# Kernel tuning notes

Measured on AMD Instinct MI355X. Metric: run time of the kernel, lower is better.

Reference implementation:

```python
import jax, jax.numpy as jnp
import numpy as np

B, N, C = 2, 100000, 256
H, D, S = 8, 64, 64
INNER = H * D

def setup_inputs() -> dict:
    key = jax.random.key(0)
    ks = jax.random.split(key, 5)
    x = jax.random.normal(ks[0], (B, N, C), dtype=jnp.float32)
    W_x = jax.random.normal(ks[1], (C, INNER), dtype=jnp.float32) / np.sqrt(C)
    b_x = jnp.zeros((INNER,), dtype=jnp.float32)
    W_fx = jax.random.normal(ks[2], (C, INNER), dtype=jnp.float32) / np.sqrt(C)
    b_fx = jnp.zeros((INNER,), dtype=jnp.float32)
    W_slice = jax.random.normal(ks[3], (D, S), dtype=jnp.float32) / np.sqrt(D)
    b_slice = jnp.zeros((S,), dtype=jnp.float32)
    temperature = jnp.ones((1, 1, H, 1), dtype=jnp.float32) * 0.5
    return {"x": x, "W_x": W_x, "b_x": b_x, "W_fx": W_fx, "b_fx": b_fx,
            "W_slice": W_slice, "b_slice": b_slice, "temperature": temperature}

def reference(x, W_x, b_x, W_fx, b_fx, W_slice, b_slice, temperature):
    b, n, _ = x.shape
    # linear projections to (B, N, H, D)
    px = (x @ W_x + b_x).reshape(b, n, H, D)   # query-like projection
    fx = (x @ W_fx + b_fx).reshape(b, n, H, D) # feature (value) projection
    # slice logits (B, N, H, S)
    slice_proj = jnp.einsum('bnhd,ds->bnhs', px, W_slice) + b_slice
    temp = jnp.clip(temperature, 0.1, 5.0)     # (1,1,H,1), broadcast over S
    slice_weights = jax.nn.softmax(slice_proj / temp, axis=-1)  # (B,N,H,S)
    slice_norm = slice_weights.sum(axis=1)     # (B,H,S)
    # weighted aggregation of tokens into slice tokens (B,H,S,D)
    slice_token = jnp.einsum('bnhs,bnhd->bhsd', slice_weights, fx)
    slice_token = slice_token / (slice_norm[..., None] + 1e-5)
    return slice_token
```

## Files before the change

### kernel.cpp

```cpp
#include <hip/hip_runtime.h>
#include <hip/hip_bf16.h>
#include <cstdint>

#define B_     2
#define N_     100000
#define C_     256
#define H_     8
#define D_     64
#define S_     64
#define INNER_ 512

#define TILE_T 64
#define NTILES ((N_ + TILE_T - 1) / TILE_T)
#define PBLK   32

#define WEFFT_OFF 0
#define WFXT_OFF  262144
#define BIASE_OFF 524288
#define SLAB_OFF  526336
#define NSLAB_OFF (SLAB_OFF + B_*H_*PBLK*4096*4)
#define WS_BIG_END (NSLAB_OFF + B_*H_*PBLK*64*4)
#define ACC_OFF   526336
#define NRM_OFF   (ACC_OFF + B_*H_*S_*D_*4)
#define WS_SMALL_END (NRM_OFF + B_*H_*S_*4)

typedef __attribute__((ext_vector_type(8))) short short8;
typedef __attribute__((ext_vector_type(4))) float f32x4;

__device__ inline short f2bf(float f) {
    __hip_bfloat16 h = __float2bfloat16(f);
    short s; __builtin_memcpy(&s, &h, 2); return s;
}
__device__ inline uint32_t pk2(float a, float b) {
    __hip_bfloat162 h = __float22bfloat162_rn(float2{a, b});
    uint32_t u; __builtin_memcpy(&u, &h, 4); return u;
}

__global__ void prep_kernel(const float* __restrict__ W_x,
                            const float* __restrict__ b_x,
                            const float* __restrict__ W_fx,
                            const float* __restrict__ W_slice,
                            const float* __restrict__ b_slice,
                            const float* __restrict__ temperature,
                            uint8_t* __restrict__ wsb) {
    int wid  = (blockIdx.x * 256 + threadIdx.x) >> 6;
    int lane = threadIdx.x & 63;
    if (wid < H_ * C_) {
        int h = wid >> 8, k = wid & 255;
        float t = temperature[h]; t = fminf(fmaxf(t, 0.1f), 5.0f);
        float sc = 1.44269504088896f / t;
        const float* wx = W_x + k * INNER_ + h * 64;
        float a = 0.f;
        #pragma unroll 8
        for (int d = 0; d < D_; ++d)
            a = fmaf(wx[d], W_slice[d * 64 + lane], a);
        ((short*)(wsb + WEFFT_OFF))[(h * 64 + lane) * 256 + k] = f2bf(a * sc);
    } else if (wid < 2 * H_ * C_) {
        int j = wid - H_ * C_;
        int h = j >> 8, k = j & 255;
        ((short*)(wsb + WFXT_OFF))[(h * 64 + lane) * 256 + k] =
            f2bf(W_fx[k * INNER_ + h * 64 + lane]);
    } else if (wid < 2 * H_ * C_ + H_) {
        int h = wid - 2 * H_ * C_;
        float t = temperature[h]; t = fminf(fmaxf(t, 0.1f), 5.0f);
        float sc = 1.44269504088896f / t;
        float a = 0.f;
        #pragma unroll 8
        for (int d = 0; d < D_; ++d)
            a = fmaf(b_x[h * 64 + d], W_slice[d * 64 + lane], a);
        ((float*)(wsb + BIASE_OFF))[h * 64 + lane] = (a + b_slice[lane]) * sc;
    }
}

template<bool SLAB>
__global__ __launch_bounds__(512, 4) void main_kernel(
        const float* __restrict__ x,
        const float* __restrict__ b_fx,
        const uint8_t* __restrict__ wsb,
        float* __restrict__ accg,
        float* __restrict__ nrmg) {
    __shared__ union {
        short xs[TILE_T * 264];
        struct { short wsl[S_ * 72]; short fsl[D_ * 72]; } wf;
    } u;
    __shared__ float smB[TILE_T * 4];

    const int tid = threadIdx.x;
    const int bid = blockIdx.x;
    const int cc = bid & 7;
    const int h  = (bid >> 3) & 7;
    const int pb = (bid >> 6) * 8 + cc;
    const int p  = pb & 31;
    const int b  = pb >> 5;

    const int lane = tid & 63, wv = tid >> 6;
    const int l = lane & 15, q = lane >> 4;
    const int g  = wv >> 2;
    const int w4 = wv & 3;

    const short* wT = (const short*)(wsb + (g ? WFXT_OFF : WEFFT_OFF)) + h * (64 * 256);
    short8 breg[8];
    #pragma unroll
    for (int k = 0; k < 8; ++k)
        breg[k] = *(const short8*)(wT + (w4 * 16 + l) * 256 + k * 32 + q * 8);

    const float bias_n = g ? b_fx[h * 64 + w4 * 16 + l]
                           : ((const float*)(wsb + BIASE_OFF))[h * 64 + w4 * 16 + l];

    const float* xb = x + (size_t)b * ((size_t)N_ * C_);
    f32x4 accO[2] = {};
    float nrmacc = 0.f;

    float4 xv[8];
    {
        const int col = lane * 4;
        #pragma unroll
        for (int j = 0; j < 8; ++j) {
            int gt = p * TILE_T + wv + 8 * j;
            xv[j] = (gt < N_) ? *(const float4*)(xb + (size_t)gt * C_ + col)
                              : float4{0.f, 0.f, 0.f, 0.f};
        }
    }

    #pragma unroll 1
    for (int tile = p; tile < NTILES; tile += PBLK) {
        __syncthreads();
        {
            #pragma unroll
            for (int j = 0; j < 8; ++j) {
                int row = wv + 8 * j;
                uint2 pk = { pk2(xv[j].x, xv[j].y), pk2(xv[j].z, xv[j].w) };
                *(uint2*)(u.xs + row * 264 + lane * 4) = pk;
            }
        }
        __syncthreads();

        {
            int nxt = tile + PBLK;
            if (nxt < NTILES) {
                const int col = lane * 4;
                #pragma unroll
                for (int j = 0; j < 8; ++j) {
                    int gt = nxt * TILE_T + wv + 8 * j;
                    xv[j] = (gt < N_) ? *(const float4*)(xb + (size_t)gt * C_ + col)
                                      : float4{0.f, 0.f, 0.f, 0.f};
                }
            }
        }

        f32x4 acc[4] = {};
        #pragma unroll
        for (int k = 0; k < 8; ++k) {
            #pragma unroll
            for (int m = 0; m < 4; ++m) {
                short8 a = *(const short8*)(u.xs + (m * 16 + l) * 264 + k * 32 + q * 8);
                acc[m] = __builtin_amdgcn_mfma_f32_16x16x32_bf16(a, breg[k], acc[m], 0, 0, 0);
            }
        }

        if (g == 0) {
            #pragma unroll
            for (int m = 0; m < 4; ++m)
                #pragma unroll
                for (int r = 0; r < 4; ++r) {
                    float e = __builtin_amdgcn_exp2f(acc[m][r] + bias_n);
                    acc[m][r] = e;
                    float sv = e;
                    sv += __shfl_xor(sv, 1, 64);
                    sv += __shfl_xor(sv, 2, 64);
                    sv += __shfl_xor(sv, 4, 64);
                    sv += __shfl_xor(sv, 8, 64);
                    if (l == 0) smB[(m * 16 + q * 4 + r) * 4 + wv] = sv;
                }
        } else {
            #pragma unroll
            for (int m = 0; m < 4; ++m)
                #pragma unroll
                for (int r = 0; r < 4; ++r)
                    acc[m][r] += bias_n;
        }
        __syncthreads();

        const int t0 = tile * TILE_T;
        if (g == 0) {
            #pragma unroll
            for (int m = 0; m < 4; ++m) {
                #pragma unroll
                for (int r = 0; r < 4; ++r) {
                    int tok = m * 16 + q * 4 + r;
                    float4 s4 = *(const float4*)(smB + tok * 4);
                    float S = (s4.x + s4.y) + (s4.z + s4.w);
                    float f = __builtin_amdgcn_rcpf(S);
                    if (t0 + tok >= N_) f = 0.f;
                    float w = acc[m][r] * f;
                    acc[m][r] = w;
                    nrmacc += w;
                }
                uint2 pk = { pk2(acc[m][0], acc[m][1]), pk2(acc[m][2], acc[m][3]) };
                *(uint2*)(u.wf.wsl + (w4 * 16 + l) * 72 + m * 16 + q * 4) = pk;
            }
        } else {
            #pragma unroll
            for (int m = 0; m < 4; ++m) {
                uint2 pk = { pk2(acc[m][0], acc[m][1]), pk2(acc[m][2], acc[m][3]) };
                *(uint2*)(u.wf.fsl + (w4 * 16 + l) * 72 + m * 16 + q * 4) = pk;
            }
        }
        __syncthreads();

        #pragma unroll
        for (int kk = 0; kk < 2; ++kk) {
            short8 aw = *(const short8*)(u.wf.wsl + (w4 * 16 + l) * 72 + kk * 32 + q * 8);
            #pragma unroll
            for (int nt = 0; nt < 2; ++nt) {
                short8 bf = *(const short8*)(u.wf.fsl + (g * 32 + nt * 16 + l) * 72 + kk * 32 + q * 8);
                accO[nt] = __builtin_amdgcn_mfma_f32_16x16x32_bf16(aw, bf, accO[nt], 0, 0, 0);
            }
        }
    }

    if (SLAB) {
        float* sp = accg + ((size_t)(b * H_ + h) * PBLK + p) * 4096;
        #pragma unroll
        for (int nt = 0; nt < 2; ++nt)
            #pragma unroll
            for (int r = 0; r < 4; ++r)
                sp[(w4 * 16 + q * 4 + r) * 64 + g * 32 + nt * 16 + l] = accO[nt][r];
        if (g == 0) {
            float v = nrmacc;
            v += __shfl_xor(v, 16, 64);
            v += __shfl_xor(v, 32, 64);
            if (lane < 16)
                nrmg[((b * H_ + h) * PBLK + p) * 64 + w4 * 16 + lane] = v;
        }
    } else {
        float* ag = accg + (size_t)((b * H_ + h) * 64) * 64;
        #pragma unroll
        for (int nt = 0; nt < 2; ++nt)
            #pragma unroll
            for (int r = 0; r < 4; ++r)
                atomicAdd(ag + (w4 * 16 + q * 4 + r) * 64 + g * 32 + nt * 16 + l, accO[nt][r]);
        if (g == 0) {
            float v = nrmacc;
            v += __shfl_xor(v, 16, 64);
            v += __shfl_xor(v, 32, 64);
            if (lane < 16)
                atomicAdd(nrmg + (b * H_ + h) * 64 + w4 * 16 + lane, v);
        }
    }
}

__global__ void finalize_big(const float* __restrict__ slab,
                             const float* __restrict__ nslab,
                             float* __restrict__ out) {
    int idx = blockIdx.x * 256 + threadIdx.x;
    int bh = idx >> 12, sd = idx & 4095, s = sd >> 6;
    const float* sp = slab  + (size_t)bh * PBLK * 4096 + sd;
    const float* np = nslab + bh * PBLK * 64 + s;
    float acc = 0.f, nn = 0.f;
    #pragma unroll 8
    for (int p = 0; p < PBLK; ++p) { acc += sp[p * 4096]; nn += np[p * 64]; }
    out[idx] = acc / (nn + 1e-5f);
}

__global__ void finalize_small(const uint8_t* __restrict__ wsb, float* __restrict__ out) {
    int idx = blockIdx.x * 256 + threadIdx.x;
    float a = ((const float*)(wsb + ACC_OFF))[idx];
    float n = ((const float*)(wsb + NRM_OFF))[idx / D_];
    out[idx] = a / (n + 1e-5f);
}

extern "C" void kernel_launch(void* const* d_in, const int* in_sizes, int n_in,
                              void* d_out, int out_size, void* d_ws, size_t ws_size,
                              hipStream_t stream) {
    const float* x           = (const float*)d_in[0];
    const float* W_x         = (const float*)d_in[1];
    const float* b_x         = (const float*)d_in[2];
    const float* W_fx        = (const float*)d_in[3];
    const float* b_fx        = (const float*)d_in[4];
    const float* W_slice     = (const float*)d_in[5];
    const float* b_slice     = (const float*)d_in[6];
    const float* temperature = (const float*)d_in[7];
    float* out = (float*)d_out;
    uint8_t* wsb = (uint8_t*)d_ws;

    int prep_waves = 2 * H_ * C_ + H_;
    prep_kernel<<<dim3((prep_waves + 3) / 4), dim3(256), 0, stream>>>(
        W_x, b_x, W_fx, W_slice, b_slice, temperature, wsb);

    if (ws_size >= (size_t)WS_BIG_END) {
        main_kernel<true><<<dim3(PBLK * H_ * B_), dim3(512), 0, stream>>>(
            x, b_fx, wsb, (float*)(wsb + SLAB_OFF), (float*)(wsb + NSLAB_OFF));
        finalize_big<<<dim3(256), dim3(256), 0, stream>>>(
            (const float*)(wsb + SLAB_OFF), (const float*)(wsb + NSLAB_OFF), out);
    } else {
        hipMemsetAsync(wsb + ACC_OFF, 0, (B_ * H_ * S_ * D_ + B_ * H_ * S_) * 4, stream);
        main_kernel<false><<<dim3(PBLK * H_ * B_), dim3(512), 0, stream>>>(
            x, b_fx, wsb, (float*)(wsb + ACC_OFF), (float*)(wsb + NRM_OFF));
        finalize_small<<<dim3(256), dim3(256), 0, stream>>>(wsb, out);
    }
}
```

Baseline: 574.9 us.

## Switch main kernel to 32x32x16 MFMA tiles with split-K output reduction

Replaces the 16x16x32 MFMA tiling with 32x32x16 MFMAs in both the projection GEMM and the slice-aggregation GEMM. Each wave now computes a 32x32 block, and the aggregation is split over K across the two wave groups, followed by an in-LDS reduction at the end. The weighted and feature slices get their own shared buffers instead of aliasing the x tile, which removes one barrier per tile. This is meant to cut LDS A-operand reads and instruction count. In exchange it uses more registers (launch bounds drop to 2 blocks per SIMD) and adds an epilogue reduction through shared memory.

```diff
diff --git a/kernel.cpp b/kernel.cpp
--- a/kernel.cpp
+++ b/kernel.cpp
@@ -24,8 +24,9 @@
 #define NRM_OFF   (ACC_OFF + B_*H_*S_*D_*4)
 #define WS_SMALL_END (NRM_OFF + B_*H_*S_*4)
 
-typedef __attribute__((ext_vector_type(8))) short short8;
-typedef __attribute__((ext_vector_type(4))) float f32x4;
+typedef __attribute__((ext_vector_type(8)))  short short8;
+typedef __attribute__((ext_vector_type(4)))  float f32x4;
+typedef __attribute__((ext_vector_type(16))) float f32x16;
 
 __device__ inline short f2bf(float f) {
     __hip_bfloat16 h = __float2bfloat16(f);
@@ -73,7 +74,7 @@
 }
 
 template<bool SLAB>
-__global__ __launch_bounds__(512, 4) void main_kernel(
+__global__ __launch_bounds__(512, 2) void main_kernel(
         const float* __restrict__ x,
         const float* __restrict__ b_fx,
         const uint8_t* __restrict__ wsb,
@@ -81,9 +82,11 @@
         float* __restrict__ nrmg) {
     __shared__ union {
         short xs[TILE_T * 264];
-        struct { short wsl[S_ * 72]; short fsl[D_ * 72]; } wf;
+        struct { float eg[4][64][16]; float np[4][64]; } fin;
     } u;
-    __shared__ float smB[TILE_T * 4];
+    __shared__ short wsl[S_ * 72];
+    __shared__ short fsl[D_ * 72];
+    __shared__ float smB[TILE_T * 2];
 
     const int tid = threadIdx.x;
     const int bid = blockIdx.x;
@@ -94,21 +97,23 @@
     const int b  = pb >> 5;
 
     const int lane = tid & 63, wv = tid >> 6;
-    const int l = lane & 15, q = lane >> 4;
+    const int l31 = lane & 31, hh = lane >> 5;
     const int g  = wv >> 2;
-    const int w4 = wv & 3;
+    const int mh = (wv >> 1) & 1;
+    const int nh = wv & 1;
+    const int kh = g, sh = mh, dh = nh;
 
     const short* wT = (const short*)(wsb + (g ? WFXT_OFF : WEFFT_OFF)) + h * (64 * 256);
-    short8 breg[8];
+    short8 breg[16];
     #pragma unroll
-    for (int k = 0; k < 8; ++k)
-        breg[k] = *(const short8*)(wT + (w4 * 16 + l) * 256 + k * 32 + q * 8);
-
-    const float bias_n = g ? b_fx[h * 64 + w4 * 16 + l]
-                           : ((const float*)(wsb + BIASE_OFF))[h * 64 + w4 * 16 + l];
+    for (int kk = 0; kk < 16; ++kk)
+        breg[kk] = *(const short8*)(wT + (nh * 32 + l31) * 256 + kk * 16 + hh * 8);
+
+    const float bias_n = g ? b_fx[h * 64 + nh * 32 + l31]
+                           : ((const float*)(wsb + BIASE_OFF))[h * 64 + nh * 32 + l31];
 
     const float* xb = x + (size_t)b * ((size_t)N_ * C_);
-    f32x4 accO[2] = {};
+    f32x16 accO = {};
     float nrmacc = 0.f;
 
     float4 xv[8];
@@ -124,14 +129,11 @@
 
     #pragma unroll 1
     for (int tile = p; tile < NTILES; tile += PBLK) {
-        __syncthreads();
-        {
-            #pragma unroll
-            for (int j = 0; j < 8; ++j) {
-                int row = wv + 8 * j;
-                uint2 pk = { pk2(xv[j].x, xv[j].y), pk2(xv[j].z, xv[j].w) };
-                *(uint2*)(u.xs + row * 264 + lane * 4) = pk;
-            }
+        #pragma unroll
+        for (int j = 0; j < 8; ++j) {
+            int row = wv + 8 * j;
+            uint2 pk = { pk2(xv[j].x, xv[j].y), pk2(xv[j].z, xv[j].w) };
+            *(uint2*)(u.xs + row * 264 + lane * 4) = pk;
         }
         __syncthreads();
 
@@ -148,105 +150,104 @@
             }
         }
 
-        f32x4 acc[4] = {};
-        #pragma unroll
-        for (int k = 0; k < 8; ++k) {
-            #pragma unroll
-            for (int m = 0; m < 4; ++m) {
-                short8 a = *(const short8*)(u.xs + (m * 16 + l) * 264 + k * 32 + q * 8);
-                acc[m] = __builtin_amdgcn_mfma_f32_16x16x32_bf16(a, breg[k], acc[m], 0, 0, 0);
-            }
+        f32x16 acc = {};
+        #pragma unroll
+        for (int kk = 0; kk < 16; ++kk) {
+            short8 a = *(const short8*)(u.xs + (mh * 32 + l31) * 264 + kk * 16 + hh * 8);
+            acc = __builtin_amdgcn_mfma_f32_32x32x16_bf16(a, breg[kk], acc, 0, 0, 0);
         }
 
         if (g == 0) {
             #pragma unroll
-            for (int m = 0; m < 4; ++m)
-                #pragma unroll
-                for (int r = 0; r < 4; ++r) {
-                    float e = __builtin_amdgcn_exp2f(acc[m][r] + bias_n);
-                    acc[m][r] = e;
-                    float sv = e;
-                    sv += __shfl_xor(sv, 1, 64);
-                    sv += __shfl_xor(sv, 2, 64);
-                    sv += __shfl_xor(sv, 4, 64);
-                    sv += __shfl_xor(sv, 8, 64);
-                    if (l == 0) smB[(m * 16 + q * 4 + r) * 4 + wv] = sv;
-                }
-        } else {
-            #pragma unroll
-            for (int m = 0; m < 4; ++m)
-                #pragma unroll
-                for (int r = 0; r < 4; ++r)
-                    acc[m][r] += bias_n;
-        }
-        __syncthreads();
-
-        const int t0 = tile * TILE_T;
-        if (g == 0) {
-            #pragma unroll
-            for (int m = 0; m < 4; ++m) {
-                #pragma unroll
-                for (int r = 0; r < 4; ++r) {
-                    int tok = m * 16 + q * 4 + r;
-                    float4 s4 = *(const float4*)(smB + tok * 4);
-                    float S = (s4.x + s4.y) + (s4.z + s4.w);
-                    float f = __builtin_amdgcn_rcpf(S);
-                    if (t0 + tok >= N_) f = 0.f;
-                    float w = acc[m][r] * f;
-                    acc[m][r] = w;
-                    nrmacc += w;
-                }
-                uint2 pk = { pk2(acc[m][0], acc[m][1]), pk2(acc[m][2], acc[m][3]) };
-                *(uint2*)(u.wf.wsl + (w4 * 16 + l) * 72 + m * 16 + q * 4) = pk;
+            for (int r = 0; r < 16; ++r) {
+                float e = __builtin_amdgcn_exp2f(acc[r] + bias_n);
+                acc[r] = e;
+                float s = e;
+                s += __shfl_xor(s, 1, 64);
+                s += __shfl_xor(s, 2, 64);
+                s += __shfl_xor(s, 4, 64);
+                s += __shfl_xor(s, 8, 64);
+                s += __shfl_xor(s, 16, 64);
+                if (l31 == 0)
+                    smB[(mh * 32 + (r & 3) + 8 * (r >> 2) + hh * 4) * 2 + nh] = s;
             }
         } else {
             #pragma unroll
-            for (int m = 0; m < 4; ++m) {
-                uint2 pk = { pk2(acc[m][0], acc[m][1]), pk2(acc[m][2], acc[m][3]) };
-                *(uint2*)(u.wf.fsl + (w4 * 16 + l) * 72 + m * 16 + q * 4) = pk;
+            for (int r = 0; r < 16; ++r) acc[r] += bias_n;
+            #pragma unroll
+            for (int rq = 0; rq < 4; ++rq) {
+                uint2 pk = { pk2(acc[rq * 4 + 0], acc[rq * 4 + 1]),
+                             pk2(acc[rq * 4 + 2], acc[rq * 4 + 3]) };
+                *(uint2*)(fsl + (nh * 32 + l31) * 72 + mh * 32 + rq * 8 + hh * 4) = pk;
             }
         }
         __syncthreads();
 
+        if (g == 0) {
+            const int t0 = tile * TILE_T;
+            #pragma unroll
+            for (int rq = 0; rq < 4; ++rq) {
+                const float* sB = smB + mh * 64 + rq * 16 + hh * 8;
+                float4 sa = *(const float4*)sB;
+                float4 sb = *(const float4*)(sB + 4);
+                float Ssum[4] = { sa.x + sa.y, sa.z + sa.w, sb.x + sb.y, sb.z + sb.w };
+                float w[4];
+                #pragma unroll
+                for (int i = 0; i < 4; ++i) {
+                    float f = __builtin_amdgcn_rcpf(Ssum[i]);
+                    int tok = mh * 32 + rq * 8 + hh * 4 + i;
+                    if (t0 + tok >= N_) f = 0.f;
+                    w[i] = acc[rq * 4 + i] * f;
+                    nrmacc += w[i];
+                }
+                uint2 pk = { pk2(w[0], w[1]), pk2(w[2], w[3]) };
+                *(uint2*)(wsl + (nh * 32 + l31) * 72 + mh * 32 + rq * 8 + hh * 4) = pk;
+            }
+        }
+        __syncthreads();
+
         #pragma unroll
         for (int kk = 0; kk < 2; ++kk) {
-            short8 aw = *(const short8*)(u.wf.wsl + (w4 * 16 + l) * 72 + kk * 32 + q * 8);
-            #pragma unroll
-            for (int nt = 0; nt < 2; ++nt) {
-                short8 bf = *(const short8*)(u.wf.fsl + (g * 32 + nt * 16 + l) * 72 + kk * 32 + q * 8);
-                accO[nt] = __builtin_amdgcn_mfma_f32_16x16x32_bf16(aw, bf, accO[nt], 0, 0, 0);
-            }
-        }
-    }
-
-    if (SLAB) {
-        float* sp = accg + ((size_t)(b * H_ + h) * PBLK + p) * 4096;
-        #pragma unroll
-        for (int nt = 0; nt < 2; ++nt)
-            #pragma unroll
-            for (int r = 0; r < 4; ++r)
-                sp[(w4 * 16 + q * 4 + r) * 64 + g * 32 + nt * 16 + l] = accO[nt][r];
-        if (g == 0) {
-            float v = nrmacc;
-            v += __shfl_xor(v, 16, 64);
-            v += __shfl_xor(v, 32, 64);
-            if (lane < 16)
-                nrmg[((b * H_ + h) * PBLK + p) * 64 + w4 * 16 + lane] = v;
+            const int tB = kh * 32 + kk * 16 + hh * 8;
+            short8 aw = *(const short8*)(wsl + (sh * 32 + l31) * 72 + tB);
+            short8 bf = *(const short8*)(fsl + (dh * 32 + l31) * 72 + tB);
+            accO = __builtin_amdgcn_mfma_f32_32x32x16_bf16(aw, bf, accO, 0, 0, 0);
+        }
+    }
+
+    if (kh == 1) {
+        const int wi = wv - 4;
+        #pragma unroll
+        for (int rq = 0; rq < 4; ++rq) {
+            f32x4 t = { accO[rq * 4 + 0], accO[rq * 4 + 1],
+                        accO[rq * 4 + 2], accO[rq * 4 + 3] };
+            *(f32x4*)&u.fin.eg[wi][lane][rq * 4] = t;
         }
     } else {
-        float* ag = accg + (size_t)((b * H_ + h) * 64) * 64;
-        #pragma unroll
-        for (int nt = 0; nt < 2; ++nt)
-            #pragma unroll
-            for (int r = 0; r < 4; ++r)
-                atomicAdd(ag + (w4 * 16 + q * 4 + r) * 64 + g * 32 + nt * 16 + l, accO[nt][r]);
-        if (g == 0) {
-            float v = nrmacc;
-            v += __shfl_xor(v, 16, 64);
-            v += __shfl_xor(v, 32, 64);
-            if (lane < 16)
-                atomicAdd(nrmg + (b * H_ + h) * 64 + w4 * 16 + lane, v);
-        }
+        u.fin.np[mh * 2 + hh][nh * 32 + l31] = nrmacc;
+    }
+    __syncthreads();
+    if (kh == 0) {
+        #pragma unroll
+        for (int r = 0; r < 16; ++r) accO[r] += u.fin.eg[wv][lane][r];
+        if (SLAB) {
+            float* sp = accg + ((size_t)(b * H_ + h) * PBLK + p) * 4096;
+            #pragma unroll
+            for (int r = 0; r < 16; ++r)
+                sp[(sh * 32 + (r & 3) + 8 * (r >> 2) + hh * 4) * 64 + dh * 32 + l31] = accO[r];
+        } else {
+            float* ag = accg + (size_t)((b * H_ + h) * 64) * 64;
+            #pragma unroll
+            for (int r = 0; r < 16; ++r)
+                atomicAdd(ag + (sh * 32 + (r & 3) + 8 * (r >> 2) + hh * 4) * 64 + dh * 32 + l31,
+                          accO[r]);
+        }
+    }
+    if (wv == 0) {
+        float v = u.fin.np[0][lane] + u.fin.np[1][lane]
+                + u.fin.np[2][lane] + u.fin.np[3][lane];
+        if (SLAB) nrmg[((b * H_ + h) * PBLK + p) * 64 + lane] = v;
+        else      atomicAdd(nrmg + (b * H_ + h) * 64 + lane, v);
     }
 }
 
```

Measured after the change: 812.2 us. +41.3%, slower.

## Retile projection GEMM to 32x32 per wave and give wsl/fsl their own shared buffers

Applied to the files above, without the earlier changes.

Each wave now computes a 32-token by 32-column block of the projection GEMM instead of 64x16, so every A fragment loaded from shared memory feeds two MFMAs. This roughly halves LDS reads per MFMA but doubles the B fragments held in registers. The wsl/fsl staging buffers move out of the union with the x tile, which removes one barrier per tile and lets the next x tile be written while the second GEMM still reads wsl/fsl. The softmax row-sum and norm reductions are reworked for the new 2x2 wave layout, with the final norm combined through shared memory. Costs are higher register use, which may cut occupancy under launch_bounds(512,4), and extra shared memory.

```diff
diff --git a/kernel.cpp b/kernel.cpp
--- a/kernel.cpp
+++ b/kernel.cpp
@@ -24,8 +24,8 @@
 #define NRM_OFF   (ACC_OFF + B_*H_*S_*D_*4)
 #define WS_SMALL_END (NRM_OFF + B_*H_*S_*4)
 
-typedef __attribute__((ext_vector_type(8))) short short8;
-typedef __attribute__((ext_vector_type(4))) float f32x4;
+typedef __attribute__((ext_vector_type(8)))  short short8;
+typedef __attribute__((ext_vector_type(4)))  float f32x4;
 
 __device__ inline short f2bf(float f) {
     __hip_bfloat16 h = __float2bfloat16(f);
@@ -81,9 +81,11 @@
         float* __restrict__ nrmg) {
     __shared__ union {
         short xs[TILE_T * 264];
-        struct { short wsl[S_ * 72]; short fsl[D_ * 72]; } wf;
+        float np[2][64];
     } u;
-    __shared__ float smB[TILE_T * 4];
+    __shared__ short wsl[S_ * 72];
+    __shared__ short fsl[D_ * 72];
+    __shared__ float smB[TILE_T * 2];
 
     const int tid = threadIdx.x;
     const int bid = blockIdx.x;
@@ -96,20 +98,29 @@
     const int lane = tid & 63, wv = tid >> 6;
     const int l = lane & 15, q = lane >> 4;
     const int g  = wv >> 2;
+    const int mh = (wv >> 1) & 1;
+    const int nh = wv & 1;
     const int w4 = wv & 3;
 
     const short* wT = (const short*)(wsb + (g ? WFXT_OFF : WEFFT_OFF)) + h * (64 * 256);
-    short8 breg[8];
+    short8 breg[2][8];
     #pragma unroll
-    for (int k = 0; k < 8; ++k)
-        breg[k] = *(const short8*)(wT + (w4 * 16 + l) * 256 + k * 32 + q * 8);
-
-    const float bias_n = g ? b_fx[h * 64 + w4 * 16 + l]
-                           : ((const float*)(wsb + BIASE_OFF))[h * 64 + w4 * 16 + l];
+    for (int j = 0; j < 2; ++j)
+        #pragma unroll
+        for (int k = 0; k < 8; ++k)
+            breg[j][k] = *(const short8*)(wT + (nh * 32 + j * 16 + l) * 256 + k * 32 + q * 8);
+
+    float bias[2];
+    {
+        const float* bp = g ? (b_fx + h * 64)
+                            : ((const float*)(wsb + BIASE_OFF) + h * 64);
+        bias[0] = bp[nh * 32 + l];
+        bias[1] = bp[nh * 32 + 16 + l];
+    }
 
     const float* xb = x + (size_t)b * ((size_t)N_ * C_);
     f32x4 accO[2] = {};
-    float nrmacc = 0.f;
+    float nrm0 = 0.f, nrm1 = 0.f;
 
     float4 xv[8];
     {
@@ -124,13 +135,81 @@
 
     #pragma unroll 1
     for (int tile = p; tile < NTILES; tile += PBLK) {
+        #pragma unroll
+        for (int j = 0; j < 8; ++j) {
+            int row = wv + 8 * j;
+            uint2 pk = { pk2(xv[j].x, xv[j].y), pk2(xv[j].z, xv[j].w) };
+            *(uint2*)(u.xs + row * 264 + lane * 4) = pk;
+        }
         __syncthreads();
-        {
-            #pragma unroll
-            for (int j = 0; j < 8; ++j) {
-                int row = wv + 8 * j;
-                uint2 pk = { pk2(xv[j].x, xv[j].y), pk2(xv[j].z, xv[j].w) };
-                *(uint2*)(u.xs + row * 264 + lane * 4) = pk;
+
+        f32x4 acc[2][2] = {};
+        #pragma unroll
+        for (int k = 0; k < 8; ++k) {
+            short8 a0 = *(const short8*)(u.xs + (mh * 32 + l) * 264 + k * 32 + q * 8);
+            short8 a1 = *(const short8*)(u.xs + (mh * 32 + 16 + l) * 264 + k * 32 + q * 8);
+            acc[0][0] = __builtin_amdgcn_mfma_f32_16x16x32_bf16(a0, breg[0][k], acc[0][0], 0, 0, 0);
+            acc[0][1] = __builtin_amdgcn_mfma_f32_16x16x32_bf16(a0, breg[1][k], acc[0][1], 0, 0, 0);
+            acc[1][0] = __builtin_amdgcn_mfma_f32_16x16x32_bf16(a1, breg[0][k], acc[1][0], 0, 0, 0);
+            acc[1][1] = __builtin_amdgcn_mfma_f32_16x16x32_bf16(a1, breg[1][k], acc[1][1], 0, 0, 0);
+        }
+
+        if (g == 0) {
+            #pragma unroll
+            for (int i = 0; i < 2; ++i)
+                #pragma unroll
+                for (int r = 0; r < 4; ++r) {
+                    float e0 = __builtin_amdgcn_exp2f(acc[i][0][r] + bias[0]);
+                    float e1 = __builtin_amdgcn_exp2f(acc[i][1][r] + bias[1]);
+                    acc[i][0][r] = e0;
+                    acc[i][1][r] = e1;
+                    float s = e0 + e1;
+                    s += __shfl_xor(s, 1, 64);
+                    s += __shfl_xor(s, 2, 64);
+                    s += __shfl_xor(s, 4, 64);
+                    s += __shfl_xor(s, 8, 64);
+                    if (l == 0) smB[(mh * 32 + i * 16 + q * 4 + r) * 2 + nh] = s;
+                }
+        } else {
+            #pragma unroll
+            for (int i = 0; i < 2; ++i) {
+                #pragma unroll
+                for (int r = 0; r < 4; ++r) {
+                    acc[i][0][r] += bias[0];
+                    acc[i][1][r] += bias[1];
+                }
+                #pragma unroll
+                for (int j = 0; j < 2; ++j) {
+                    uint2 pk = { pk2(acc[i][j][0], acc[i][j][1]),
+                                 pk2(acc[i][j][2], acc[i][j][3]) };
+                    *(uint2*)(fsl + (nh * 32 + j * 16 + l) * 72 + mh * 32 + i * 16 + q * 4) = pk;
+                }
+            }
+        }
+        __syncthreads();
+
+        if (g == 0) {
+            const int t0 = tile * TILE_T;
+            #pragma unroll
+            for (int i = 0; i < 2; ++i) {
+                const int tb = mh * 32 + i * 16 + q * 4;
+                float4 fa = *(const float4*)(smB + tb * 2);
+                float4 fb = *(const float4*)(smB + tb * 2 + 4);
+                float Ss[4] = { fa.x + fa.y, fa.z + fa.w, fb.x + fb.y, fb.z + fb.w };
+                float w0[4], w1[4];
+                #pragma unroll
+                for (int r = 0; r < 4; ++r) {
+                    float f = __builtin_amdgcn_rcpf(Ss[r]);
+                    if (t0 + tb + r >= N_) f = 0.f;
+                    w0[r] = acc[i][0][r] * f;
+                    w1[r] = acc[i][1][r] * f;
+                    nrm0 += w0[r];
+                    nrm1 += w1[r];
+                }
+                uint2 p0 = { pk2(w0[0], w0[1]), pk2(w0[2], w0[3]) };
+                uint2 p1 = { pk2(w1[0], w1[1]), pk2(w1[2], w1[3]) };
+                *(uint2*)(wsl + (nh * 32 + l) * 72      + tb) = p0;
+                *(uint2*)(wsl + (nh * 32 + 16 + l) * 72 + tb) = p1;
             }
         }
         __syncthreads();
@@ -148,77 +227,30 @@
             }
         }
 
-        f32x4 acc[4] = {};
-        #pragma unroll
-        for (int k = 0; k < 8; ++k) {
-            #pragma unroll
-            for (int m = 0; m < 4; ++m) {
-                short8 a = *(const short8*)(u.xs + (m * 16 + l) * 264 + k * 32 + q * 8);
-                acc[m] = __builtin_amdgcn_mfma_f32_16x16x32_bf16(a, breg[k], acc[m], 0, 0, 0);
-            }
-        }
-
-        if (g == 0) {
-            #pragma unroll
-            for (int m = 0; m < 4; ++m)
-                #pragma unroll
-                for (int r = 0; r < 4; ++r) {
-                    float e = __builtin_amdgcn_exp2f(acc[m][r] + bias_n);
-                    acc[m][r] = e;
-                    float sv = e;
-                    sv += __shfl_xor(sv, 1, 64);
-                    sv += __shfl_xor(sv, 2, 64);
-                    sv += __shfl_xor(sv, 4, 64);
-                    sv += __shfl_xor(sv, 8, 64);
-                    if (l == 0) smB[(m * 16 + q * 4 + r) * 4 + wv] = sv;
-                }
-        } else {
-            #pragma unroll
-            for (int m = 0; m < 4; ++m)
-                #pragma unroll
-                for (int r = 0; r < 4; ++r)
-                    acc[m][r] += bias_n;
-        }
-        __syncthreads();
-
-        const int t0 = tile * TILE_T;
-        if (g == 0) {
-            #pragma unroll
-            for (int m = 0; m < 4; ++m) {
-                #pragma unroll
-                for (int r = 0; r < 4; ++r) {
-                    int tok = m * 16 + q * 4 + r;
-                    float4 s4 = *(const float4*)(smB + tok * 4);
-                    float S = (s4.x + s4.y) + (s4.z + s4.w);
-                    float f = __builtin_amdgcn_rcpf(S);
-                    if (t0 + tok >= N_) f = 0.f;
-                    float w = acc[m][r] * f;
-                    acc[m][r] = w;
-                    nrmacc += w;
-                }
-                uint2 pk = { pk2(acc[m][0], acc[m][1]), pk2(acc[m][2], acc[m][3]) };
-                *(uint2*)(u.wf.wsl + (w4 * 16 + l) * 72 + m * 16 + q * 4) = pk;
-            }
-        } else {
-            #pragma unroll
-            for (int m = 0; m < 4; ++m) {
-                uint2 pk = { pk2(acc[m][0], acc[m][1]), pk2(acc[m][2], acc[m][3]) };
-                *(uint2*)(u.wf.fsl + (w4 * 16 + l) * 72 + m * 16 + q * 4) = pk;
-            }
-        }
-        __syncthreads();
-
         #pragma unroll
         for (int kk = 0; kk < 2; ++kk) {
-            short8 aw = *(const short8*)(u.wf.wsl + (w4 * 16 + l) * 72 + kk * 32 + q * 8);
+            short8 aw = *(const short8*)(wsl + (w4 * 16 + l) * 72 + kk * 32 + q * 8);
             #pragma unroll
             for (int nt = 0; nt < 2; ++nt) {
-                short8 bf = *(const short8*)(u.wf.fsl + (g * 32 + nt * 16 + l) * 72 + kk * 32 + q * 8);
+                short8 bf = *(const short8*)(fsl + (g * 32 + nt * 16 + l) * 72 + kk * 32 + q * 8);
                 accO[nt] = __builtin_amdgcn_mfma_f32_16x16x32_bf16(aw, bf, accO[nt], 0, 0, 0);
             }
         }
     }
 
+    __syncthreads();
+    if (g == 0) {
+        nrm0 += __shfl_xor(nrm0, 16, 64);
+        nrm0 += __shfl_xor(nrm0, 32, 64);
+        nrm1 += __shfl_xor(nrm1, 16, 64);
+        nrm1 += __shfl_xor(nrm1, 32, 64);
+        if (lane < 16) {
+            u.np[mh][nh * 32 + lane]      = nrm0;
+            u.np[mh][nh * 32 + 16 + lane] = nrm1;
+        }
+    }
+    __syncthreads();
+
     if (SLAB) {
         float* sp = accg + ((size_t)(b * H_ + h) * PBLK + p) * 4096;
         #pragma unroll
@@ -226,12 +258,9 @@
             #pragma unroll
             for (int r = 0; r < 4; ++r)
                 sp[(w4 * 16 + q * 4 + r) * 64 + g * 32 + nt * 16 + l] = accO[nt][r];
-        if (g == 0) {
-            float v = nrmacc;
-            v += __shfl_xor(v, 16, 64);
-            v += __shfl_xor(v, 32, 64);
-            if (lane < 16)
-                nrmg[((b * H_ + h) * PBLK + p) * 64 + w4 * 16 + lane] = v;
+        if (wv == 0) {
+            float v = u.np[0][lane] + u.np[1][lane];
+            nrmg[((b * H_ + h) * PBLK + p) * 64 + lane] = v;
         }
     } else {
         float* ag = accg + (size_t)((b * H_ + h) * 64) * 64;
@@ -240,12 +269,9 @@
             #pragma unroll
             for (int r = 0; r < 4; ++r)
                 atomicAdd(ag + (w4 * 16 + q * 4 + r) * 64 + g * 32 + nt * 16 + l, accO[nt][r]);
-        if (g == 0) {
-            float v = nrmacc;
-            v += __shfl_xor(v, 16, 64);
-            v += __shfl_xor(v, 32, 64);
-            if (lane < 16)
-                atomicAdd(nrmg + (b * H_ + h) * 64 + w4 * 16 + lane, v);
+        if (wv == 0) {
+            float v = u.np[0][lane] + u.np[1][lane];
+            atomicAdd(nrmg + (b * H_ + h) * 64 + lane, v);
         }
     }
 }
```

After: 769.0 us. 1.34x slower.
